# Performance work log

Hardware: AMD Instinct MI355X
Metric: run time of the kernel (lower is better)

## Reference

```python
import jax, jax.numpy as jnp
import numpy as np
from jax import lax

D_MODEL = 1024
N_HEADS = 8
D_HEAD = 64
D_INNER = N_HEADS * D_HEAD  # 512
B, T = 4, 4096
LN_EPS = 1e-5
NORM_EPS = 1e-12  # F.normalize default eps


def setup_inputs() -> dict:
    key = jax.random.key(0)
    ks = jax.random.split(key, 6)
    s_proj = (2.0 / (D_MODEL + D_INNER)) ** 0.5  # xavier_uniform-ish std
    x = jax.random.normal(ks[0], (B, T, D_MODEL), jnp.float32)
    Wq = jax.random.normal(ks[1], (D_MODEL, D_INNER), jnp.float32) * s_proj
    Wk = jax.random.normal(ks[2], (D_MODEL, D_INNER), jnp.float32) * s_proj
    Wv = jax.random.normal(ks[3], (D_MODEL, D_INNER), jnp.float32) * s_proj
    Wa = jax.random.normal(ks[4], (D_MODEL, D_INNER), jnp.float32) * s_proj
    ba = jnp.full((D_INNER,), 3.0, jnp.float32)  # nn.init.constant_(W_alpha.bias, 3.0)
    Wo = jax.random.normal(ks[5], (D_INNER, D_MODEL), jnp.float32) * s_proj
    gamma = jnp.ones((D_MODEL,), jnp.float32)
    beta = jnp.zeros((D_MODEL,), jnp.float32)
    return {"x": x, "Wq": Wq, "Wk": Wk, "Wv": Wv, "Wa": Wa, "ba": ba,
            "Wo": Wo, "gamma": gamma, "beta": beta}


def reference(x, Wq, Wk, Wv, Wa, ba, Wo, gamma, beta):
    Bx, Tx, _ = x.shape
    residual = x
    # LayerNorm
    mu = jnp.mean(x, axis=-1, keepdims=True)
    var = jnp.var(x, axis=-1, keepdims=True)
    xn = (x - mu) / jnp.sqrt(var + LN_EPS) * gamma + beta
    # Projections -> (B, T, H, d) -> time-major (T, B, H, d) for scan
    def heads(y):
        return jnp.moveaxis(y.reshape(Bx, Tx, N_HEADS, D_HEAD), 1, 0)
    q = heads(xn @ Wq)
    k = heads(xn @ Wk)
    v = heads(xn @ Wv)
    alpha = jax.nn.sigmoid(heads(xn @ Wa + ba))
    # F.normalize(k, dim=-1)
    knorm = jnp.linalg.norm(k, axis=-1, keepdims=True)
    k = k / jnp.maximum(knorm, NORM_EPS)

    # Recurrence: S_t = diag(a_t) S_{t-1} + k_t v_t^T ; o_t = S_t^T q_t
    def step(S, inp):
        q_t, k_t, v_t, a_t = inp  # each (B, H, d)
        S = a_t[..., None] * S + k_t[..., None] * v_t[..., None, :]  # (B,H,dk,dv)
        o_t = jnp.einsum('bhji,bhj->bhi', S, q_t)
        return S, o_t

    S0 = jnp.zeros((Bx, N_HEADS, D_HEAD, D_HEAD), x.dtype)
    _, outs = lax.scan(step, S0, (q, k, v, alpha))  # outs: (T, B, H, d)
    out = jnp.moveaxis(outs, 0, 1).reshape(Bx, Tx, D_INNER) @ Wo
    return out + residual
```

## Files before the change

kernel.cpp:

```cpp
#include <hip/hip_runtime.h>
#include <stdint.h>

#define NTOK   16384
#define DM     1024
#define DI     512
#define NH     8
#define DH     64
#define CHUNK  64
#define NCH    64
#define NBHC   2048

using short8 = __attribute__((ext_vector_type(8))) short;
using f32x4  = __attribute__((ext_vector_type(4))) float;

__device__ __forceinline__ unsigned short f2bf(float f) {
  union { float f; unsigned int u; } x; x.f = f;
  unsigned int u = x.u;
  return (unsigned short)((u + 0x7fffu + ((u >> 16) & 1u)) >> 16);
}
__device__ __forceinline__ float bf2f(unsigned short h) {
  union { unsigned int u; float f; } x; x.u = ((unsigned int)h) << 16; return x.f;
}

typedef const __attribute__((address_space(1))) void* gp1_t;
typedef __attribute__((address_space(3))) void* lp3_t;
__device__ __forceinline__ void gload_lds16(const void* g, void* l) {
  __builtin_amdgcn_global_load_lds((gp1_t)g, (lp3_t)l, 16, 0, 0);
}

__global__ __launch_bounds__(256) void transpose4_bf16(const float* __restrict__ Wq,
                                                       const float* __restrict__ Wk,
                                                       const float* __restrict__ Wv,
                                                       const float* __restrict__ Wa,
                                                       unsigned short* __restrict__ out) {
  const int z = blockIdx.z;
  const float* in = (z == 0) ? Wq : (z == 1) ? Wk : (z == 2) ? Wv : Wa;
  unsigned short* o = out + (size_t)z * 512 * 1024;
  __shared__ float tile[32][33];
  int bx = blockIdx.x * 32;
  int by = blockIdx.y * 32;
  int tx = threadIdx.x & 31, ty = threadIdx.x >> 5;
  #pragma unroll
  for (int r = ty; r < 32; r += 8) tile[r][tx] = in[(long)(by + r) * 512 + bx + tx];
  __syncthreads();
  #pragma unroll
  for (int r = ty; r < 32; r += 8) o[(long)(bx + r) * 1024 + by + tx] = f2bf(tile[tx][r]);
}

__global__ __launch_bounds__(256) void transpose_bf16(const float* __restrict__ in,
                                                      unsigned short* __restrict__ out,
                                                      int R, int C) {
  __shared__ float tile[32][33];
  int bx = blockIdx.x * 32;
  int by = blockIdx.y * 32;
  int tx = threadIdx.x & 31, ty = threadIdx.x >> 5;
  #pragma unroll
  for (int r = ty; r < 32; r += 8) tile[r][tx] = in[(long)(by + r) * C + bx + tx];
  __syncthreads();
  #pragma unroll
  for (int r = ty; r < 32; r += 8) out[(long)(bx + r) * R + by + tx] = f2bf(tile[tx][r]);
}

__global__ __launch_bounds__(256) void ln_kernel(const float* __restrict__ x,
                                                 const float* __restrict__ gamma,
                                                 const float* __restrict__ beta,
                                                 unsigned short* __restrict__ xn) {
  const int row = blockIdx.x, tid = threadIdx.x;
  float4 v = ((const float4*)(x + (long)row * DM))[tid];
  float s  = v.x + v.y + v.z + v.w;
  float ss = v.x * v.x + v.y * v.y + v.z * v.z + v.w * v.w;
  #pragma unroll
  for (int off = 32; off > 0; off >>= 1) { s += __shfl_down(s, off); ss += __shfl_down(ss, off); }
  __shared__ float rs_[4], rss_[4];
  int wave = tid >> 6, lane = tid & 63;
  if (lane == 0) { rs_[wave] = s; rss_[wave] = ss; }
  __syncthreads();
  s  = rs_[0] + rs_[1] + rs_[2] + rs_[3];
  ss = rss_[0] + rss_[1] + rss_[2] + rss_[3];
  float mu   = s * (1.f / DM);
  float var  = ss * (1.f / DM) - mu * mu;
  float rstd = rsqrtf(var + 1e-5f);
  int idx = tid * 4;
  float xv[4] = {v.x, v.y, v.z, v.w};
  unsigned short o[4];
  #pragma unroll
  for (int j = 0; j < 4; ++j) o[j] = f2bf((xv[j] - mu) * rstd * gamma[idx + j] + beta[idx + j]);
  uint2 pk; pk.x = (unsigned)o[0] | ((unsigned)o[1] << 16); pk.y = (unsigned)o[2] | ((unsigned)o[3] << 16);
  *(uint2*)(xn + (long)row * DM + idx) = pk;
}

#define EPS 136
template <int MODE>
__global__ __launch_bounds__(512) void gemm_bt(const unsigned short* __restrict__ A,
                                               const unsigned short* __restrict__ Bt,
                                               unsigned short* __restrict__ Cb,
                                               float* __restrict__ Cf,
                                               const float* __restrict__ resid,
                                               int M, int N, int K) {
  __shared__ __align__(16) unsigned short smem[128 * EPS];
  unsigned short* As = smem;
  unsigned short* Bs = smem + 8192;
  const int tid = threadIdx.x;
  const int wave = tid >> 6, lane = tid & 63;
  const int quad = lane >> 4, l16 = lane & 15;

  const int Nt = gridDim.y;
  int id = blockIdx.x + blockIdx.y * gridDim.x;
  int group = id / (4 * Nt);
  int rem = id - group * (4 * Nt);
  const int m0 = (group * 4 + (rem & 3)) * 256;
  const int n0 = (rem >> 2) * 128;
  const int wm = (wave & 3) * 64, wn = (wave >> 2) * 64;

  const int r4 = tid >> 2, p4 = (tid & 3) * 8;
  const unsigned short* Ag0 = A + (long)(m0 + r4) * K + p4;
  const unsigned short* Ag1 = A + (long)(m0 + 128 + r4) * K + p4;
  const unsigned short* Bg0 = Bt + (long)(n0 + r4) * K + p4;

  f32x4 acc[4][4];
  #pragma unroll
  for (int i = 0; i < 4; ++i)
    #pragma unroll
    for (int j = 0; j < 4; ++j) acc[i][j] = (f32x4){0.f, 0.f, 0.f, 0.f};

  for (int k0 = 0; k0 < K; k0 += 32) {
    __syncthreads();
    gload_lds16(Ag0 + k0, &As[tid * 8]);
    gload_lds16(Ag1 + k0, &As[(tid + 512) * 8]);
    gload_lds16(Bg0 + k0, &Bs[tid * 8]);
    __syncthreads();
    short8 a[4], b[4];
    #pragma unroll
    for (int mt = 0; mt < 4; ++mt) a[mt] = *(const short8*)&As[(wm + mt * 16 + l16) * 32 + quad * 8];
    #pragma unroll
    for (int nt = 0; nt < 4; ++nt) b[nt] = *(const short8*)&Bs[(wn + nt * 16 + l16) * 32 + quad * 8];
    #pragma unroll
    for (int mt = 0; mt < 4; ++mt)
      #pragma unroll
      for (int nt = 0; nt < 4; ++nt)
        acc[mt][nt] = __builtin_amdgcn_mfma_f32_16x16x32_bf16(a[mt], b[nt], acc[mt][nt], 0, 0, 0);
  }
  unsigned short* epi = smem;
  const int mypass = (wave & 3) >> 1;
  const int rloc = ((wave & 1) * 64);
  #pragma unroll
  for (int h = 0; h < 2; ++h) {
    __syncthreads();
    if (mypass == h) {
      #pragma unroll
      for (int mt = 0; mt < 4; ++mt)
        #pragma unroll
        for (int nt = 0; nt < 4; ++nt)
          #pragma unroll
          for (int r = 0; r < 4; ++r)
            epi[(rloc + mt * 16 + quad * 4 + r) * EPS + wn + nt * 16 + l16] = f2bf(acc[mt][nt][r]);
    }
    __syncthreads();
    if (MODE == 0) {
      #pragma unroll
      for (int i = tid; i < 2048; i += 512) {
        int row = i >> 4, cc = (i & 15) * 8;
        uint4 v = *(const uint4*)&epi[row * EPS + cc];
        *(uint4*)&Cb[(long)(m0 + h * 128 + row) * N + n0 + cc] = v;
      }
    } else {
      #pragma unroll
      for (int i = tid; i < 4096; i += 512) {
        int row = i >> 5, cc = (i & 31) * 4;
        long g = (long)(m0 + h * 128 + row) * N + n0 + cc;
        float4 rv = *(const float4*)&resid[g];
        uint2 pv = *(const uint2*)&epi[row * EPS + cc];
        float4 ov;
        ov.x = bf2f((unsigned short)(pv.x & 0xffffu)) + rv.x;
        ov.y = bf2f((unsigned short)(pv.x >> 16))     + rv.y;
        ov.z = bf2f((unsigned short)(pv.y & 0xffffu)) + rv.z;
        ov.w = bf2f((unsigned short)(pv.y >> 16))     + rv.w;
        *(float4*)&Cf[g] = ov;
      }
    }
  }
}

#define TS 72
__global__ __launch_bounds__(256) void prep_intra_kernel(const unsigned short* __restrict__ Cb,
                                                         const float* __restrict__ ba,
                                                         unsigned short* __restrict__ qt,
                                                         float* __restrict__ Dvec,
                                                         unsigned short* __restrict__ Ointra,
                                                         unsigned short* __restrict__ Tt) {
  const int bhc = blockIdx.x;
  const int c = bhc & 63, bh = bhc >> 6;
  const int h = bh & 7, b = bh >> 3;
  const int tid = threadIdx.x;
  __shared__ __align__(16) unsigned short Qb[4096], Kb[4096];
  __shared__ __align__(16) unsigned short Vt[64 * TS], Ht[64 * TS];
  __shared__ float lamF[4096];
  __shared__ float rnF[64];
  const long rowbase = ((long)(b * 4096 + c * 64)) * 2048;
  const int hoff = h * 64;

  if (tid < 64) rnF[tid] = 0.f;
  __syncthreads();

  #pragma unroll
  for (int chunk = 0; chunk < 2; ++chunk) {
    int u = chunk * 256 + tid;
    int t = u >> 3, p = u & 7;
    long g = rowbase + (long)t * 2048 + hoff + p * 8;
    uint4 q4 = *(const uint4*)(Cb + g);
    uint4 k4 = *(const uint4*)(Cb + g + 512);
    uint4 v4 = *(const uint4*)(Cb + g + 1024);
    uint4 a4 = *(const uint4*)(Cb + g + 1536);
    *(uint4*)&Qb[u * 8] = q4;
    *(uint4*)&Kb[u * 8] = k4;
    const unsigned short* vs = (const unsigned short*)&v4;
    #pragma unroll
    for (int j = 0; j < 8; ++j) Vt[(p * 8 + j) * TS + t] = vs[j];
    const unsigned short* as_ = (const unsigned short*)&a4;
    #pragma unroll
    for (int j = 0; j < 8; ++j) {
      float z = bf2f(as_[j]) + ba[hoff + p * 8 + j];
      lamF[t * 64 + p * 8 + j] = 1.f / (1.f + __expf(-z));
    }
    const unsigned short* ks = (const unsigned short*)&k4;
    float ssq = 0.f;
    #pragma unroll
    for (int j = 0; j < 8; ++j) { float kv = bf2f(ks[j]); ssq += kv * kv; }
    atomicAdd(&rnF[t], ssq);
  }
  __syncthreads();

  if (tid < 64) {
    int d = tid; float cum = 1.f;
    #pragma unroll
    for (int t = 0; t < 64; ++t) { cum *= lamF[t * 64 + d]; lamF[t * 64 + d] = cum; }
    Dvec[(long)bhc * 64 + d] = cum;
  } else if (tid < 128) {
    int t = tid - 64;
    rnF[t] = 1.f / fmaxf(sqrtf(rnF[t]), 1e-12f);
  }
  __syncthreads();

  {
    const int d = tid & 63;
    const float lend = lamF[63 * 64 + d];
    #pragma unroll
    for (int j = 0; j < 16; ++j) {
      int e = j * 256 + tid;
      int t = e >> 6;
      float lam = lamF[e];
      float rl = 1.f / lam;
      float kn = bf2f(Kb[e]) * rnF[t];
      Qb[e] = f2bf(bf2f(Qb[e]) * lam);
      Kb[e] = f2bf(kn * rl);
      Ht[d * TS + t] = f2bf(kn * lend * rl);
    }
  }
  __syncthreads();

  {
    const long obase = (long)bhc * 4096;
    uint4* gq = (uint4*)(qt + obase);
    const uint4* lq = (const uint4*)Qb;
    gq[tid] = lq[tid]; gq[tid + 256] = lq[tid + 256];
  }

  const long base = (long)bhc * 4096;
  const int wave = tid >> 6, lane = tid & 63, quad = lane >> 4, l16 = lane & 15;
  const int mrow = wave * 16 + l16;
  unsigned short* Ps = (unsigned short*)lamF;

  {
    short8 a0 = *(const short8*)&Qb[mrow * 64 + quad * 8];
    short8 a1 = *(const short8*)&Qb[mrow * 64 + 32 + quad * 8];
    #pragma unroll
    for (int nt = 0; nt < 4; ++nt) {
      short8 b0 = *(const short8*)&Kb[(nt * 16 + l16) * 64 + quad * 8];
      short8 b1 = *(const short8*)&Kb[(nt * 16 + l16) * 64 + 32 + quad * 8];
      f32x4 acc = (f32x4){0.f, 0.f, 0.f, 0.f};
      acc = __builtin_amdgcn_mfma_f32_16x16x32_bf16(a0, b0, acc, 0, 0, 0);
      acc = __builtin_amdgcn_mfma_f32_16x16x32_bf16(a1, b1, acc, 0, 0, 0);
      #pragma unroll
      for (int r = 0; r < 4; ++r) {
        int t = wave * 16 + quad * 4 + r, u = nt * 16 + l16;
        Ps[t * 64 + u] = (u <= t) ? f2bf(acc[r]) : (unsigned short)0;
      }
    }
  }
  {
    short8 a0 = *(const short8*)&Ps[mrow * 64 + quad * 8];
    short8 a1 = *(const short8*)&Ps[mrow * 64 + 32 + quad * 8];
    #pragma unroll
    for (int nt = 0; nt < 4; ++nt) {
      short8 b0 = *(const short8*)&Vt[(nt * 16 + l16) * TS + quad * 8];
      short8 b1 = *(const short8*)&Vt[(nt * 16 + l16) * TS + 32 + quad * 8];
      f32x4 acc = (f32x4){0.f, 0.f, 0.f, 0.f};
      acc = __builtin_amdgcn_mfma_f32_16x16x32_bf16(a0, b0, acc, 0, 0, 0);
      acc = __builtin_amdgcn_mfma_f32_16x16x32_bf16(a1, b1, acc, 0, 0, 0);
      #pragma unroll
      for (int r = 0; r < 4; ++r) {
        int t = wave * 16 + quad * 4 + r, i = nt * 16 + l16;
        Ointra[base + t * 64 + i] = f2bf(acc[r]);
      }
    }
  }
  {
    short8 a0 = *(const short8*)&Vt[mrow * TS + quad * 8];
    short8 a1 = *(const short8*)&Vt[mrow * TS + 32 + quad * 8];
    #pragma unroll
    for (int nt = 0; nt < 4; ++nt) {
      short8 b0 = *(const short8*)&Ht[(nt * 16 + l16) * TS + quad * 8];
      short8 b1 = *(const short8*)&Ht[(nt * 16 + l16) * TS + 32 + quad * 8];
      f32x4 acc = (f32x4){0.f, 0.f, 0.f, 0.f};
      acc = __builtin_amdgcn_mfma_f32_16x16x32_bf16(a0, b0, acc, 0, 0, 0);
      acc = __builtin_amdgcn_mfma_f32_16x16x32_bf16(a1, b1, acc, 0, 0, 0);
      #pragma unroll
      for (int r = 0; r < 4; ++r) {
        int i = wave * 16 + quad * 4 + r, j = nt * 16 + l16;
        Tt[base + i * 64 + j] = f2bf(acc[r]);
      }
    }
  }
}

__global__ __launch_bounds__(256) void scan_kernel(const unsigned short* __restrict__ Tt,
                                                   const float* __restrict__ Dvec,
                                                   unsigned short* __restrict__ Sst) {
  const int bh = blockIdx.x;
  const int e = blockIdx.y * 256 + threadIdx.x;
  const int j = e & 63;
  float S = 0.f;
  for (int c = 0; c < 64; ++c) {
    const long idx = ((long)(bh * 64 + c)) * 4096 + e;
    const float dj = Dvec[((long)(bh * 64 + c)) * 64 + j];
    Sst[idx] = f2bf(S);
    S = dj * S + bf2f(Tt[idx]);
  }
}

__global__ __launch_bounds__(256) void combine_kernel(const unsigned short* __restrict__ qt,
                                                      const unsigned short* __restrict__ Sst,
                                                      const unsigned short* __restrict__ Ointra,
                                                      unsigned short* __restrict__ O) {
  const int bhc = blockIdx.x;
  const int c = bhc & 63, bh = bhc >> 6;
  const int h = bh & 7, b = bh >> 3;
  const long base = (long)bhc * 4096;
  __shared__ __align__(16) unsigned short Qs[4096], Sb[4096];
  const int tid = threadIdx.x;
  {
    const uint4* gq = (const uint4*)(qt + base);  uint4* lq = (uint4*)Qs;
    const uint4* gs = (const uint4*)(Sst + base); uint4* ls = (uint4*)Sb;
    lq[tid] = gq[tid]; lq[tid + 256] = gq[tid + 256];
    ls[tid] = gs[tid]; ls[tid + 256] = gs[tid + 256];
  }
  __syncthreads();
  const int wave = tid >> 6, lane = tid & 63, quad = lane >> 4, l16 = lane & 15;
  const int mrow = wave * 16 + l16;
  short8 a0 = *(const short8*)&Qs[mrow * 64 + quad * 8];
  short8 a1 = *(const short8*)&Qs[mrow * 64 + 32 + quad * 8];
  #pragma unroll
  for (int nt = 0; nt < 4; ++nt) {
    f32x4 acc;
    #pragma unroll
    for (int r = 0; r < 4; ++r) {
      int t = wave * 16 + quad * 4 + r, i = nt * 16 + l16;
      acc[r] = bf2f(Ointra[base + t * 64 + i]);
    }
    short8 b0 = *(const short8*)&Sb[(nt * 16 + l16) * 64 + quad * 8];
    short8 b1 = *(const short8*)&Sb[(nt * 16 + l16) * 64 + 32 + quad * 8];
    acc = __builtin_amdgcn_mfma_f32_16x16x32_bf16(a0, b0, acc, 0, 0, 0);
    acc = __builtin_amdgcn_mfma_f32_16x16x32_bf16(a1, b1, acc, 0, 0, 0);
    #pragma unroll
    for (int r = 0; r < 4; ++r) {
      int t = wave * 16 + quad * 4 + r, i = nt * 16 + l16;
      O[((long)(b * 4096 + c * 64 + t)) * 512 + h * 64 + i] = f2bf(acc[r]);
    }
  }
}

extern "C" void kernel_launch(void* const* d_in, const int* in_sizes, int n_in,
                              void* d_out, int out_size, void* d_ws, size_t ws_size,
                              hipStream_t stream) {
  const float* x     = (const float*)d_in[0];
  const float* Wq    = (const float*)d_in[1];
  const float* Wk    = (const float*)d_in[2];
  const float* Wv    = (const float*)d_in[3];
  const float* Wa    = (const float*)d_in[4];
  const float* ba    = (const float*)d_in[5];
  const float* Wo    = (const float*)d_in[6];
  const float* gamma = (const float*)d_in[7];
  const float* beta  = (const float*)d_in[8];
  float* out = (float*)d_out;

  char* ws = (char*)d_ws;
  const size_t KB = 1024;
  unsigned short* Wt     = (unsigned short*)(ws + 0 * KB);
  unsigned short* Wot    = (unsigned short*)(ws + 4096 * KB);
  float*          Dvec   = (float*)         (ws + 5120 * KB);
  unsigned short* qt     = (unsigned short*)(ws + 5632 * KB);
  unsigned short* Ttb    = (unsigned short*)(ws + 22016 * KB);
  unsigned short* Sst    = (unsigned short*)(ws + 38400 * KB);
  unsigned short* xn     = (unsigned short*)(ws + 54784 * KB);
  unsigned short* Ointra = (unsigned short*)(ws + 54784 * KB);
  unsigned short* Ob     = (unsigned short*)(ws + 71168 * KB);
  unsigned short* Cb     = (unsigned short*)(ws + 87552 * KB);

  transpose4_bf16<<<dim3(16, 32, 4), 256, 0, stream>>>(Wq, Wk, Wv, Wa, Wt);
  transpose_bf16<<<dim3(32, 16), 256, 0, stream>>>(Wo, Wot, 512, 1024);
  ln_kernel<<<NTOK, 256, 0, stream>>>(x, gamma, beta, xn);
  gemm_bt<0><<<dim3(NTOK / 256, 2048 / 128), 512, 0, stream>>>(xn, Wt, Cb, nullptr, nullptr, NTOK, 2048, 1024);
  prep_intra_kernel<<<NBHC, 256, 0, stream>>>(Cb, ba, qt, Dvec, Ointra, Ttb);
  scan_kernel<<<dim3(32, 16), 256, 0, stream>>>(Ttb, Dvec, Sst);
  combine_kernel<<<NBHC, 256, 0, stream>>>(qt, Sst, Ointra, Ob);
  gemm_bt<1><<<dim3(NTOK / 256, 1024 / 128), 512, 0, stream>>>(Ob, Wot, nullptr, out, x, NTOK, 1024, 512);
}
```

Before: 311.0 us.

## Merge prep launches and transpose V/K in LDS via identity MFMA

The LayerNorm kernel and both weight-transpose kernels are merged into one launch, with block ranges assigned to each job, to save launch overhead. In prep_intra, the cumulative-decay buffer now stays in bf16 instead of fp32, which reduces LDS use. V and normalized K are transposed into LDS by multiplying with an identity matrix on the MFMA units, replacing scalar scattered LDS writes, and the chunk-end decay factor is applied at the Tt store instead of in a separate Ht buffer. In exchange, the cumulative decay is rounded to bf16 (less precise) and an extra barrier plus MFMA pass is added.

Result: no change. 305.8 us (-1.7%).

```diff
diff --git a/kernel.cpp b/kernel.cpp
--- a/kernel.cpp
+++ b/kernel.cpp
@@ -28,65 +28,64 @@
   __builtin_amdgcn_global_load_lds((gp1_t)g, (lp3_t)l, 16, 0, 0);
 }
 
-__global__ __launch_bounds__(256) void transpose4_bf16(const float* __restrict__ Wq,
-                                                       const float* __restrict__ Wk,
-                                                       const float* __restrict__ Wv,
-                                                       const float* __restrict__ Wa,
-                                                       unsigned short* __restrict__ out) {
-  const int z = blockIdx.z;
-  const float* in = (z == 0) ? Wq : (z == 1) ? Wk : (z == 2) ? Wv : Wa;
-  unsigned short* o = out + (size_t)z * 512 * 1024;
+__global__ __launch_bounds__(256) void init_kernel(const float* __restrict__ x,
+                                                   const float* __restrict__ gamma,
+                                                   const float* __restrict__ beta,
+                                                   const float* __restrict__ Wq,
+                                                   const float* __restrict__ Wk,
+                                                   const float* __restrict__ Wv,
+                                                   const float* __restrict__ Wa,
+                                                   const float* __restrict__ Wo,
+                                                   unsigned short* __restrict__ xn,
+                                                   unsigned short* __restrict__ Wt,
+                                                   unsigned short* __restrict__ Wot) {
+  const int blk = blockIdx.x, tid = threadIdx.x;
   __shared__ float tile[32][33];
-  int bx = blockIdx.x * 32;
-  int by = blockIdx.y * 32;
-  int tx = threadIdx.x & 31, ty = threadIdx.x >> 5;
-  #pragma unroll
-  for (int r = ty; r < 32; r += 8) tile[r][tx] = in[(long)(by + r) * 512 + bx + tx];
-  __syncthreads();
-  #pragma unroll
-  for (int r = ty; r < 32; r += 8) o[(long)(bx + r) * 1024 + by + tx] = f2bf(tile[tx][r]);
-}
-
-__global__ __launch_bounds__(256) void transpose_bf16(const float* __restrict__ in,
-                                                      unsigned short* __restrict__ out,
-                                                      int R, int C) {
-  __shared__ float tile[32][33];
-  int bx = blockIdx.x * 32;
-  int by = blockIdx.y * 32;
-  int tx = threadIdx.x & 31, ty = threadIdx.x >> 5;
-  #pragma unroll
-  for (int r = ty; r < 32; r += 8) tile[r][tx] = in[(long)(by + r) * C + bx + tx];
-  __syncthreads();
-  #pragma unroll
-  for (int r = ty; r < 32; r += 8) out[(long)(bx + r) * R + by + tx] = f2bf(tile[tx][r]);
-}
-
-__global__ __launch_bounds__(256) void ln_kernel(const float* __restrict__ x,
-                                                 const float* __restrict__ gamma,
-                                                 const float* __restrict__ beta,
-                                                 unsigned short* __restrict__ xn) {
-  const int row = blockIdx.x, tid = threadIdx.x;
-  float4 v = ((const float4*)(x + (long)row * DM))[tid];
-  float s  = v.x + v.y + v.z + v.w;
-  float ss = v.x * v.x + v.y * v.y + v.z * v.z + v.w * v.w;
-  #pragma unroll
-  for (int off = 32; off > 0; off >>= 1) { s += __shfl_down(s, off); ss += __shfl_down(ss, off); }
   __shared__ float rs_[4], rss_[4];
-  int wave = tid >> 6, lane = tid & 63;
-  if (lane == 0) { rs_[wave] = s; rss_[wave] = ss; }
-  __syncthreads();
-  s  = rs_[0] + rs_[1] + rs_[2] + rs_[3];
-  ss = rss_[0] + rss_[1] + rss_[2] + rss_[3];
-  float mu   = s * (1.f / DM);
-  float var  = ss * (1.f / DM) - mu * mu;
-  float rstd = rsqrtf(var + 1e-5f);
-  int idx = tid * 4;
-  float xv[4] = {v.x, v.y, v.z, v.w};
-  unsigned short o[4];
-  #pragma unroll
-  for (int j = 0; j < 4; ++j) o[j] = f2bf((xv[j] - mu) * rstd * gamma[idx + j] + beta[idx + j]);
-  uint2 pk; pk.x = (unsigned)o[0] | ((unsigned)o[1] << 16); pk.y = (unsigned)o[2] | ((unsigned)o[3] << 16);
-  *(uint2*)(xn + (long)row * DM + idx) = pk;
+  if (blk < NTOK) {
+    const int row = blk;
+    float4 v = ((const float4*)(x + (long)row * DM))[tid];
+    float s  = v.x + v.y + v.z + v.w;
+    float ss = v.x * v.x + v.y * v.y + v.z * v.z + v.w * v.w;
+    #pragma unroll
+    for (int off = 32; off > 0; off >>= 1) { s += __shfl_down(s, off); ss += __shfl_down(ss, off); }
+    int wave = tid >> 6, lane = tid & 63;
+    if (lane == 0) { rs_[wave] = s; rss_[wave] = ss; }
+    __syncthreads();
+    s  = rs_[0] + rs_[1] + rs_[2] + rs_[3];
+    ss = rss_[0] + rss_[1] + rss_[2] + rss_[3];
+    float mu   = s * (1.f / DM);
+    float var  = ss * (1.f / DM) - mu * mu;
+    float rstd = rsqrtf(var + 1e-5f);
+    int idx = tid * 4;
+    float xv[4] = {v.x, v.y, v.z, v.w};
+    unsigned short o[4];
+    #pragma unroll
+    for (int j = 0; j < 4; ++j) o[j] = f2bf((xv[j] - mu) * rstd * gamma[idx + j] + beta[idx + j]);
+    uint2 pk; pk.x = (unsigned)o[0] | ((unsigned)o[1] << 16); pk.y = (unsigned)o[2] | ((unsigned)o[3] << 16);
+    *(uint2*)(xn + (long)row * DM + idx) = pk;
+  } else if (blk < NTOK + 2048) {
+    const int id = blk - NTOK;
+    const int z = id >> 9, r9 = id & 511;
+    const float* in = (z == 0) ? Wq : (z == 1) ? Wk : (z == 2) ? Wv : Wa;
+    unsigned short* o = Wt + (size_t)z * 512 * 1024;
+    int bx = (r9 & 15) * 32, by = (r9 >> 4) * 32;
+    int tx = tid & 31, ty = tid >> 5;
+    #pragma unroll
+    for (int r = ty; r < 32; r += 8) tile[r][tx] = in[(long)(by + r) * 512 + bx + tx];
+    __syncthreads();
+    #pragma unroll
+    for (int r = ty; r < 32; r += 8) o[(long)(bx + r) * 1024 + by + tx] = f2bf(tile[tx][r]);
+  } else {
+    const int id = blk - NTOK - 2048;
+    int bx = (id & 31) * 32, by = (id >> 5) * 32;
+    int tx = tid & 31, ty = tid >> 5;
+    #pragma unroll
+    for (int r = ty; r < 32; r += 8) tile[r][tx] = Wo[(long)(by + r) * 1024 + bx + tx];
+    __syncthreads();
+    #pragma unroll
+    for (int r = ty; r < 32; r += 8) Wot[(long)(bx + r) * 512 + by + tx] = f2bf(tile[tx][r]);
+  }
 }
 
 #define EPS 136
@@ -192,10 +191,9 @@
   const int c = bhc & 63, bh = bhc >> 6;
   const int h = bh & 7, b = bh >> 3;
   const int tid = threadIdx.x;
-  __shared__ __align__(16) unsigned short Qb[4096], Kb[4096];
-  __shared__ __align__(16) unsigned short Vt[64 * TS], Ht[64 * TS];
-  __shared__ float lamF[4096];
-  __shared__ float rnF[64];
+  __shared__ __align__(16) unsigned short Qb[4096], Kb[4096], Vb[4096], lamB[4096];
+  __shared__ __align__(16) unsigned short Vt[64 * TS], Kt[64 * TS];
+  __shared__ float rnF[64], lendF[64];
   const long rowbase = ((long)(b * 4096 + c * 64)) * 2048;
   const int hoff = h * 64;
 
@@ -213,15 +211,18 @@
     uint4 a4 = *(const uint4*)(Cb + g + 1536);
     *(uint4*)&Qb[u * 8] = q4;
     *(uint4*)&Kb[u * 8] = k4;
-    const unsigned short* vs = (const unsigned short*)&v4;
-    #pragma unroll
-    for (int j = 0; j < 8; ++j) Vt[(p * 8 + j) * TS + t] = vs[j];
+    *(uint4*)&Vb[u * 8] = v4;
     const unsigned short* as_ = (const unsigned short*)&a4;
+    unsigned short al[8];
     #pragma unroll
     for (int j = 0; j < 8; ++j) {
       float z = bf2f(as_[j]) + ba[hoff + p * 8 + j];
-      lamF[t * 64 + p * 8 + j] = 1.f / (1.f + __expf(-z));
-    }
+      al[j] = f2bf(1.f / (1.f + __expf(-z)));
+    }
+    uint4 pa;
+    pa.x = (unsigned)al[0] | ((unsigned)al[1] << 16); pa.y = (unsigned)al[2] | ((unsigned)al[3] << 16);
+    pa.z = (unsigned)al[4] | ((unsigned)al[5] << 16); pa.w = (unsigned)al[6] | ((unsigned)al[7] << 16);
+    *(uint4*)&lamB[u * 8] = pa;
     const unsigned short* ks = (const unsigned short*)&k4;
     float ssq = 0.f;
     #pragma unroll
@@ -233,28 +234,26 @@
   if (tid < 64) {
     int d = tid; float cum = 1.f;
     #pragma unroll
-    for (int t = 0; t < 64; ++t) { cum *= lamF[t * 64 + d]; lamF[t * 64 + d] = cum; }
+    for (int t = 0; t < 64; ++t) {
+      cum *= bf2f(lamB[t * 64 + d]);
+      lamB[t * 64 + d] = f2bf(cum);
+    }
     Dvec[(long)bhc * 64 + d] = cum;
+    lendF[d] = cum;
   } else if (tid < 128) {
     int t = tid - 64;
     rnF[t] = 1.f / fmaxf(sqrtf(rnF[t]), 1e-12f);
   }
   __syncthreads();
 
-  {
-    const int d = tid & 63;
-    const float lend = lamF[63 * 64 + d];
-    #pragma unroll
-    for (int j = 0; j < 16; ++j) {
-      int e = j * 256 + tid;
-      int t = e >> 6;
-      float lam = lamF[e];
-      float rl = 1.f / lam;
-      float kn = bf2f(Kb[e]) * rnF[t];
-      Qb[e] = f2bf(bf2f(Qb[e]) * lam);
-      Kb[e] = f2bf(kn * rl);
-      Ht[d * TS + t] = f2bf(kn * lend * rl);
-    }
+  #pragma unroll
+  for (int j = 0; j < 16; ++j) {
+    int e = j * 256 + tid;
+    int t = e >> 6;
+    float lam = bf2f(lamB[e]);
+    float kn = bf2f(Kb[e]) * rnF[t];
+    Qb[e] = f2bf(bf2f(Qb[e]) * lam);
+    Kb[e] = f2bf(kn / lam);
   }
   __syncthreads();
 
@@ -268,7 +267,15 @@
   const long base = (long)bhc * 4096;
   const int wave = tid >> 6, lane = tid & 63, quad = lane >> 4, l16 = lane & 15;
   const int mrow = wave * 16 + l16;
-  unsigned short* Ps = (unsigned short*)lamF;
+  unsigned short* Ps = lamB;
+
+  union { short8 v; short s[8]; } aI;
+  aI.v = (short8){0,0,0,0,0,0,0,0};
+  {
+    int target = ((wave & 1) * 16 + l16) - quad * 8;
+    if (target >= 0 && target < 8) aI.s[target] = (short)0x3F80;
+  }
+  const int bsel = (wave >> 1) * 32;
 
   {
     short8 a0 = *(const short8*)&Qb[mrow * 64 + quad * 8];
@@ -287,6 +294,23 @@
       }
     }
   }
+  #pragma unroll
+  for (int nt = 0; nt < 4; ++nt) {
+    short8 bv = *(const short8*)&Vb[(nt * 16 + l16) * 64 + bsel + quad * 8];
+    short8 bk = *(const short8*)&Kb[(nt * 16 + l16) * 64 + bsel + quad * 8];
+    f32x4 av = (f32x4){0.f, 0.f, 0.f, 0.f};
+    f32x4 ak = (f32x4){0.f, 0.f, 0.f, 0.f};
+    av = __builtin_amdgcn_mfma_f32_16x16x32_bf16(aI.v, bv, av, 0, 0, 0);
+    ak = __builtin_amdgcn_mfma_f32_16x16x32_bf16(aI.v, bk, ak, 0, 0, 0);
+    #pragma unroll
+    for (int r = 0; r < 4; ++r) {
+      int i = wave * 16 + quad * 4 + r, t = nt * 16 + l16;
+      Vt[i * TS + t] = f2bf(av[r]);
+      Kt[i * TS + t] = f2bf(ak[r]);
+    }
+  }
+  __syncthreads();
+
   {
     short8 a0 = *(const short8*)&Ps[mrow * 64 + quad * 8];
     short8 a1 = *(const short8*)&Ps[mrow * 64 + 32 + quad * 8];
@@ -309,15 +333,16 @@
     short8 a1 = *(const short8*)&Vt[mrow * TS + 32 + quad * 8];
     #pragma unroll
     for (int nt = 0; nt < 4; ++nt) {
-      short8 b0 = *(const short8*)&Ht[(nt * 16 + l16) * TS + quad * 8];
-      short8 b1 = *(const short8*)&Ht[(nt * 16 + l16) * TS + 32 + quad * 8];
+      short8 b0 = *(const short8*)&Kt[(nt * 16 + l16) * TS + quad * 8];
+      short8 b1 = *(const short8*)&Kt[(nt * 16 + l16) * TS + 32 + quad * 8];
       f32x4 acc = (f32x4){0.f, 0.f, 0.f, 0.f};
       acc = __builtin_amdgcn_mfma_f32_16x16x32_bf16(a0, b0, acc, 0, 0, 0);
       acc = __builtin_amdgcn_mfma_f32_16x16x32_bf16(a1, b1, acc, 0, 0, 0);
+      float le = lendF[nt * 16 + l16];
       #pragma unroll
       for (int r = 0; r < 4; ++r) {
         int i = wave * 16 + quad * 4 + r, j = nt * 16 + l16;
-        Tt[base + i * 64 + j] = f2bf(acc[r]);
+        Tt[base + i * 64 + j] = f2bf(acc[r] * le);
       }
     }
   }
@@ -406,9 +431,7 @@
   unsigned short* Ob     = (unsigned short*)(ws + 71168 * KB);
   unsigned short* Cb     = (unsigned short*)(ws + 87552 * KB);
 
-  transpose4_bf16<<<dim3(16, 32, 4), 256, 0, stream>>>(Wq, Wk, Wv, Wa, Wt);
-  transpose_bf16<<<dim3(32, 16), 256, 0, stream>>>(Wo, Wot, 512, 1024);
-  ln_kernel<<<NTOK, 256, 0, stream>>>(x, gamma, beta, xn);
+  init_kernel<<<NTOK + 2048 + 512, 256, 0, stream>>>(x, gamma, beta, Wq, Wk, Wv, Wa, Wo, xn, Wt, Wot);
   gemm_bt<0><<<dim3(NTOK / 256, 2048 / 128), 512, 0, stream>>>(xn, Wt, Cb, nullptr, nullptr, NTOK, 2048, 1024);
   prep_intra_kernel<<<NBHC, 256, 0, stream>>>(Cb, ba, qt, Dvec, Ointra, Ttb);
   scan_kernel<<<dim3(32, 16), 256, 0, stream>>>(Ttb, Dvec, Sst);
```
